# Optimization experiments

Hardware: AMD Instinct MI355X
Metric: run time of the kernel (lower is better)

## Reference

```python
import math
import jax, jax.numpy as jnp
import numpy as np

# Gemma4Audio config constants
HID = 1024
H = 8
D = HID // H            # 128
CHUNK = 12              # attention_chunk_size
PAST = 13 - 1           # max_past_horizon = context_left - 1
FUT = 0                 # max_future_horizon = context_right
CTX = CHUNK + PAST + FUT  # 24
SOFTCAP = 50.0
Q_SCALE = D ** (-0.5) / math.log(2)
K_SCALE = math.log(1.0 + math.e) / math.log(2)


def setup_inputs() -> dict:
    key = jax.random.key(0)
    ks = jax.random.split(key, 8)
    B, S = 4, 6144
    P = CTX + 1  # 25 relative positions
    std = HID ** (-0.5)
    return {
        "hidden_states": jax.random.normal(ks[0], (B, S, HID), jnp.float32),
        "position_embeddings": jax.random.normal(ks[1], (P, HID), jnp.float32),
        "Wq": jax.random.normal(ks[2], (HID, HID), jnp.float32) * std,
        "Wk": jax.random.normal(ks[3], (HID, HID), jnp.float32) * std,
        "Wv": jax.random.normal(ks[4], (HID, HID), jnp.float32) * std,
        "Wpost": jax.random.normal(ks[5], (HID, HID), jnp.float32) * std,
        "Wrel": jax.random.normal(ks[6], (HID, HID), jnp.float32) * std,
        "per_dim_scale": jnp.zeros((D,), jnp.float32),  # torch init: zeros
    }


def _extract_block_context(x, num_blocks):
    # x: [B, S, H, D] -> [B, num_blocks, CTX, H, D]
    xp = jnp.pad(x, ((0, 0), (PAST, FUT + CHUNK - 1), (0, 0), (0, 0)))
    idx = jnp.arange(num_blocks)[:, None] * CHUNK + jnp.arange(CTX)[None, :]
    return xp[:, idx]  # gather along seq axis


def _rel_shift(x):
    # x: [B, H, nb, CHUNK, P] -> [B, H, nb, CHUNK, CTX]
    B, Hh, nb, bs, pos_len = x.shape
    x = jnp.pad(x, ((0, 0), (0, 0), (0, 0), (0, 0), (0, CTX + 1 - pos_len)))
    x = x.reshape(B, Hh, nb, bs * (CTX + 1))[..., : bs * CTX]
    return x.reshape(B, Hh, nb, bs, CTX)


def reference(hidden_states, position_embeddings, Wq, Wk, Wv, Wpost, Wrel, per_dim_scale):
    B, S, _ = hidden_states.shape
    nb = (S + CHUNK - 1) // CHUNK
    pad = nb * CHUNK - S

    # Projections (ClippableLinear clamps are +/-inf at init -> identity)
    q = (hidden_states @ Wq.T).reshape(B, S, H, D)
    k = (hidden_states @ Wk.T).reshape(B, S, H, D)
    v = (hidden_states @ Wv.T).reshape(B, S, H, D)

    q = q * (Q_SCALE * jax.nn.softplus(per_dim_scale))  # per-dim scaled queries
    k = k * K_SCALE

    # [B, nb, CHUNK, H, D]
    q_blocked = jnp.pad(q, ((0, 0), (0, pad), (0, 0), (0, 0))).reshape(B, nb, CHUNK, H, D)
    k_ctx = _extract_block_context(k, nb)  # [B, nb, CTX, H, D]
    v_ctx = _extract_block_context(v, nb)

    # content score: [B, H, nb, CHUNK, CTX]
    matrix_ac = jnp.einsum('bnchd,bnkhd->bhnck', q_blocked, k_ctx)

    # relative position score
    rel_k = (position_embeddings @ Wrel.T).reshape(-1, H, D)  # [P, H, D]
    matrix_bd = jnp.einsum('bnchd,phd->bhncp', q_blocked, rel_k)
    matrix_bd = _rel_shift(matrix_bd)  # [B, H, nb, CHUNK, CTX]

    logits = matrix_ac + matrix_bd
    logits = jnp.tanh(logits / SOFTCAP) * SOFTCAP  # softcap
    attn = jax.nn.softmax(logits, axis=-1)

    out = jnp.einsum('bhnck,bnkhd->bnchd', attn, v_ctx)
    out = out.reshape(B, nb * CHUNK, H * D)[:, :S]
    return out @ Wpost.T
```

## Files before the change

kernel.cpp:

```cpp
#include <hip/hip_runtime.h>
#include <hip/hip_bf16.h>
#include <math.h>

typedef unsigned short ushort_t;
typedef __attribute__((ext_vector_type(8))) short short8;
typedef __attribute__((ext_vector_type(4))) short s4v;
typedef __attribute__((ext_vector_type(4))) float float4v;

#define HID 1024
#define NH 8
#define DH 128
#define CHUNK 12
#define PAST 12
#define CTX 24
#define NPOS 25
#define QKVW 3072

__device__ __forceinline__ float bf2f(ushort_t b){
  union{unsigned int u; float f;} x; x.u = ((unsigned int)b)<<16; return x.f;
}
__device__ __forceinline__ ushort_t f2bf(float f){
  union{float f; unsigned int u;} x; x.f = f;
  unsigned int u = x.u;
  unsigned int r = u + 0x7fffu + ((u>>16)&1u);
  return (ushort_t)(r>>16);
}

__device__ __forceinline__ void gload16(const ushort_t* g, ushort_t* l){
  __builtin_amdgcn_global_load_lds(
      (const __attribute__((address_space(1))) unsigned int*)g,
      (__attribute__((address_space(3))) unsigned int*)l,
      16, 0, 0);
}

__global__ __launch_bounds__(256) void cvt_all(
    const float* __restrict__ hs, const float* __restrict__ Wq,
    const float* __restrict__ Wk, const float* __restrict__ Wv,
    const float* __restrict__ Wp, ushort_t* __restrict__ hsb,
    ushort_t* __restrict__ Wcat, ushort_t* __restrict__ Wpb, int nhs4)
{
  const int W4 = 262144;
  const int total = nhs4 + 4*W4;
  for (int i = blockIdx.x*256 + threadIdx.x; i < total; i += gridDim.x*256){
    const float4v* src; s4v* dst; int off;
    if (i < nhs4){ src = (const float4v*)hs; dst = (s4v*)hsb; off = i; }
    else {
      int j = i - nhs4; int seg = j >> 18; off = j & (W4-1);
      src = (const float4v*)(seg==0?Wq:seg==1?Wk:seg==2?Wv:Wp);
      dst = (seg<3) ? ((s4v*)Wcat) + (size_t)seg*W4 : (s4v*)Wpb;
    }
    float4v v = src[off];
    s4v o;
#pragma unroll
    for (int j2=0;j2<4;j2++) o[j2] = (short)f2bf(v[j2]);
    dst[off] = o;
  }
}

template<int MODE, int OUTF>
__global__ __launch_bounds__(256) void gemm3(
    const ushort_t* __restrict__ A, const ushort_t* __restrict__ W,
    void* __restrict__ Cv, int M, int N, int K,
    const float* __restrict__ pds, float qsc, float ksc)
{
  const int nwg  = gridDim.x;
  const int orig = blockIdx.x;
  const int qch  = nwg >> 3, rch = nwg & 7;
  const int xcd  = orig & 7, idx = orig >> 3;
  const int bid  = (xcd < rch ? xcd*(qch+1) : rch*(qch+1) + (xcd-rch)*qch) + idx;

  const int NT = N >> 7;
  const int m0 = (bid / NT) * 128;
  const int n0 = (bid % NT) * 128;

  const int tid  = threadIdx.x;
  const int w    = tid >> 6, lane = tid & 63;
  const int wm   = w >> 1, wn = w & 1;
  const int lr   = lane & 15;
  const int lg   = lane >> 4;

  __shared__ ushort_t slab[6*128*32];
  ushort_t* a0 = slab;                 ushort_t* b0 = slab + 128*32;
  ushort_t* a1 = slab + 2*128*32;      ushort_t* b1 = slab + 3*128*32;
  ushort_t* a2 = slab + 4*128*32;      ushort_t* b2 = slab + 5*128*32;

  float4v acc[4][4];
#pragma unroll
  for (int i=0;i<4;i++)
#pragma unroll
    for (int j=0;j<4;j++) acc[i][j] = (float4v)0.0f;

  const int sr = ((lane >> 3) << 1) | ((lane >> 2) & 1);
  const int sc = ((lane & 3) ^ ((lane >> 3) & 3)) * 8;

  const int fidx = ((lr >> 1)*8 + (lr & 1)*4 + (lg ^ ((lr >> 1) & 3))) * 8;

  const ushort_t* Ab0 = A + (size_t)(m0 + w*16      + sr)*K + sc;
  const ushort_t* Ab1 = A + (size_t)(m0 + 64 + w*16 + sr)*K + sc;
  const ushort_t* Bb0 = W + (size_t)(n0 + w*16      + sr)*K + sc;
  const ushort_t* Bb1 = W + (size_t)(n0 + 64 + w*16 + sr)*K + sc;

#define STAGE(Abuf, Bbuf, kt) do {                    \
    gload16(Ab0 + (kt), &(Abuf)[(w*16)*32]);          \
    gload16(Ab1 + (kt), &(Abuf)[(64 + w*16)*32]);     \
    gload16(Bb0 + (kt), &(Bbuf)[(w*16)*32]);          \
    gload16(Bb1 + (kt), &(Bbuf)[(64 + w*16)*32]);     \
  } while(0)

#define COMPUTE(Abuf, Bbuf) do {                                             \
    short8 afr[4], bfr[4];                                                   \
    _Pragma("unroll")                                                        \
    for (int i=0;i<4;i++) afr[i] = *(const short8*)&(Abuf)[(wm*4 + i)*512 + fidx]; \
    _Pragma("unroll")                                                        \
    for (int j=0;j<4;j++) bfr[j] = *(const short8*)&(Bbuf)[(wn*4 + j)*512 + fidx]; \
    __builtin_amdgcn_s_setprio(1);                                           \
    _Pragma("unroll")                                                        \
    for (int i=0;i<4;i++)                                                    \
      _Pragma("unroll")                                                      \
      for (int j=0;j<4;j++)                                                  \
        acc[i][j] = __builtin_amdgcn_mfma_f32_16x16x32_bf16(afr[i], bfr[j], acc[i][j], 0,0,0); \
    __builtin_amdgcn_s_setprio(0);                                           \
  } while(0)

  const int nt = K >> 5;
  STAGE(a0, b0, 0);
  STAGE(a1, b1, 32);

  for (int t = 0; t < nt; ++t){
    if (t == nt-1) asm volatile("s_waitcnt vmcnt(0)" ::: "memory");
    else           asm volatile("s_waitcnt vmcnt(4)" ::: "memory");
    asm volatile("s_barrier" ::: "memory");
    if (t+2 < nt) STAGE(a2, b2, (t+2)*32);
    COMPUTE(a0, b0);
    ushort_t* ta = a0; a0 = a1; a1 = a2; a2 = ta;
    ushort_t* tb = b0; b0 = b1; b1 = b2; b2 = tb;
  }
#undef STAGE
#undef COMPUTE

  __syncthreads();

  if (OUTF == 0){
#pragma unroll
    for (int j=0;j<4;j++){
      const int col = wn*64 + j*16 + lr;
      float scale = 1.0f;
      if (MODE==1){
        const int gcol = n0 + col;
        if (gcol < 1024){ float p = pds[gcol & (DH-1)]; scale = qsc * log1pf(expf(p)); }
        else if (gcol < 2048) scale = ksc;
      }
#pragma unroll
      for (int i=0;i<4;i++){
        const int row = wm*64 + i*16 + lg*4;
#pragma unroll
        for (int r=0;r<4;r++)
          slab[(row + r)*128 + col] = f2bf(acc[i][j][r] * scale);
      }
    }
    __syncthreads();
    ushort_t* Crow = (ushort_t*)Cv + (size_t)m0*N + n0;
    const int rr = tid >> 4, sl = (tid & 15)*8;
#pragma unroll
    for (int it=0; it<8; ++it){
      const int row = it*16 + rr;
      *(short8*)&Crow[(size_t)row*N + sl] = *(const short8*)&slab[row*128 + sl];
    }
  } else {
    float* smf = (float*)slab;
    float* Crow = (float*)Cv + (size_t)m0*N + n0;
#pragma unroll
    for (int h2=0; h2<2; ++h2){
      __syncthreads();
      if (wm == h2){
#pragma unroll
        for (int j=0;j<4;j++){
          const int col = wn*64 + j*16 + lr;
#pragma unroll
          for (int i=0;i<4;i++){
            const int row = i*16 + lg*4;
#pragma unroll
            for (int r=0;r<4;r++)
              smf[(row + r)*128 + col] = acc[i][j][r];
          }
        }
      }
      __syncthreads();
      const int rr = tid >> 5, half = ((tid >> 4) & 1)*64, sl = (tid & 15)*4;
#pragma unroll
      for (int it=0; it<8; ++it){
        const int row = it*8 + rr;
        *(float4v*)&Crow[(size_t)(h2*64 + row)*N + half + sl] =
            *(const float4v*)&smf[row*128 + half + sl];
      }
    }
  }
}

__global__ __launch_bounds__(256) void relk2(
    const float* __restrict__ pe, const float* __restrict__ Wrel,
    ushort_t* __restrict__ rel)
{
  int g = blockIdx.x*256 + threadIdx.x;
  int idx = g >> 1, par = g & 1;
  if (idx >= NPOS*HID) return;
  int p = idx >> 10, n = idx & 1023;
  const float* a = pe + p*HID + par*512;
  const float* w = Wrel + (size_t)n*HID + par*512;
  float s = 0.f;
  for (int k=0;k<512;k+=4){
    float4v av = *(const float4v*)(a+k);
    float4v wv = *(const float4v*)(w+k);
#pragma unroll
    for (int u=0;u<4;u++) s += av[u]*wv[u];
  }
  s += __shfl_xor(s, 1, 64);
  if (!par) rel[idx] = f2bf(s);
}

__global__ __launch_bounds__(256) void attn_kernel(
  const ushort_t* __restrict__ qkv, const ushort_t* __restrict__ rel,
  ushort_t* __restrict__ o, int S)
{
  const int n0 = blockIdx.x * 4;
  const int b  = blockIdx.y, h = blockIdx.z;
  const int tid = threadIdx.x;
  const size_t bS = (size_t)b * S;

  __shared__ ushort_t lds[24800];
  ushort_t* ks = lds;
  ushort_t* vt = lds + 9248;
  float*    sB = (float*)(lds + 17952);
  ushort_t* rs = lds + 20448;
  float*    sA = (float*)(lds + 20448);

  const int base = n0*CHUNK - PAST;
  {
    const int r0 = tid >> 4;
    const int c0 = (tid & 15) * 8;
    for (int r = r0; r < 68; r += 16){
      int s = base + r;
      short8 kv = (short8)0, vv = (short8)0;
      if (r < 60 && s >= 0 && s < S){
        kv = *(const short8*)&qkv[(bS + s)*QKVW + 1024 + h*DH + c0];
        vv = *(const short8*)&qkv[(bS + s)*QKVW + 2048 + h*DH + c0];
      }
      *(short8*)&ks[r*136 + c0] = kv;
#pragma unroll
      for (int u=0;u<8;u++) vt[(c0+u)*68 + r] = (ushort_t)vv[u];
    }
    for (int r = r0; r < 32; r += 16){
      short8 rv = (short8)0;
      if (r < NPOS) rv = *(const short8*)&rel[r*HID + h*DH + c0];
      *(short8*)&rs[r*136 + c0] = rv;
    }
  }
  __syncthreads();

  const int w    = tid >> 6;
  const int lane = tid & 63;
  const int lr   = lane & 15;
  const int lg   = lane >> 4;

  float*    sAw = sA + w*312;
  float*    sBw = sB + w*312;
  ushort_t* Ppw = lds + w*640;

  int qrow = (n0 + w)*CHUNK + lr;
  if (qrow >= S) qrow = S - 1;
  const ushort_t* qp = qkv + (bS + qrow)*QKVW + h*DH + lg*8;
  short8 qf[4];
#pragma unroll
  for (int ks2=0; ks2<4; ks2++) qf[ks2] = *(const short8*)(qp + ks2*32);

#pragma unroll
  for (int t0=0; t0<2; t0++){
    float4v acc = (float4v)0.0f;
#pragma unroll
    for (int ks2=0; ks2<4; ks2++){
      short8 rf = *(const short8*)&rs[(t0*16 + lr)*136 + ks2*32 + lg*8];
      acc = __builtin_amdgcn_mfma_f32_16x16x32_bf16(qf[ks2], rf, acc, 0,0,0);
    }
    const int p = t0*16 + lr;
#pragma unroll
    for (int reg=0; reg<4; reg++){
      int cr = lg*4 + reg;
      if (cr < CHUNK && p < NPOS) sBw[cr*26 + p] = acc[reg];
    }
  }
  __syncthreads();

#pragma unroll
  for (int t0=0; t0<2; t0++){
    float4v acc = (float4v)0.0f;
#pragma unroll
    for (int ks2=0; ks2<4; ks2++){
      short8 kf = *(const short8*)&ks[(w*CHUNK + t0*16 + lr)*136 + ks2*32 + lg*8];
      acc = __builtin_amdgcn_mfma_f32_16x16x32_bf16(qf[ks2], kf, acc, 0,0,0);
    }
    const int t = t0*16 + lr;
#pragma unroll
    for (int reg=0; reg<4; reg++){
      int cr = lg*4 + reg;
      if (cr < CHUNK && t < CTX) sAw[cr*26 + t] = acc[reg];
    }
  }
  __syncthreads();

  if (lane < CHUNK) *(short8*)&Ppw[lane*40 + 24] = (short8)0;

  {
    const int c2 = lane >> 5;
    const int t  = lane & 31;
#pragma unroll
    for (int i=0;i<6;i++){
      int c = i*2 + c2;
      float x = -1e30f;
      if (t < CTX){
        int f = c*CTX + t;
        int r = f / NPOS, p = f - r*NPOS;
        x = sAw[c*26 + t] + sBw[r*26 + p];
        x = 50.0f * tanhf(x * 0.02f);
      }
      float m = x;
      for (int off=16; off>=1; off>>=1) m = fmaxf(m, __shfl_xor(m, off, 32));
      float e = (t < CTX) ? expf(x - m) : 0.0f;
      float s = e;
      for (int off=16; off>=1; off>>=1) s += __shfl_xor(s, off, 32);
      if (t < CTX) Ppw[c*40 + t] = f2bf(e / s);
    }
  }

  short8 pf = *(const short8*)&Ppw[lr*40 + lg*8];
  const int orow_base = (n0 + w)*CHUNK;
#pragma unroll
  for (int j=0; j<8; j++){
    int d  = j*16 + lr;
    int tb = w*CHUNK + lg*8;
    s4v b0 = *(const s4v*)&vt[d*68 + tb];
    s4v b1 = *(const s4v*)&vt[d*68 + tb + 4];
    short8 bf;
#pragma unroll
    for (int u=0;u<4;u++){ bf[u] = b0[u]; bf[u+4] = b1[u]; }
    float4v a = __builtin_amdgcn_mfma_f32_16x16x32_bf16(pf, bf, (float4v)0.0f, 0,0,0);
#pragma unroll
    for (int reg=0; reg<4; reg++){
      int cr = lg*4 + reg;
      if (cr < CHUNK)
        o[(bS + orow_base + cr)*HID + h*DH + j*16 + lr] = f2bf(a[reg]);
    }
  }
}

extern "C" void kernel_launch(void* const* d_in, const int* in_sizes, int n_in,
                              void* d_out, int out_size, void* d_ws, size_t ws_size,
                              hipStream_t stream)
{
  const float* hs    = (const float*)d_in[0];
  const float* pe    = (const float*)d_in[1];
  const float* Wq    = (const float*)d_in[2];
  const float* Wk    = (const float*)d_in[3];
  const float* Wv    = (const float*)d_in[4];
  const float* Wpost = (const float*)d_in[5];
  const float* Wrel  = (const float*)d_in[6];
  const float* pds   = (const float*)d_in[7];
  float* out = (float*)d_out;

  const int BS = in_sizes[0] / HID;
  const int B  = 4;
  const int S  = BS / B;
  const int nb = S / CHUNK;

  const size_t per = (size_t)BS * HID;
  const size_t wsz = (size_t)HID * HID;
  ushort_t* qkv  = (ushort_t*)d_ws;
  ushort_t* at   = qkv  + (size_t)BS * QKVW;
  ushort_t* rel  = at   + per;
  ushort_t* hsb  = rel  + (size_t)NPOS*HID;
  ushort_t* Wcat = hsb  + per;
  ushort_t* Wpb  = Wcat + 3*wsz;

  const float qsc = (float)(pow((double)DH, -0.5) / log(2.0));
  const float ksc = (float)(log(1.0 + exp(1.0)) / log(2.0));

  cvt_all<<<4096, 256, 0, stream>>>(hs, Wq, Wk, Wv, Wpost, hsb, Wcat, Wpb,
                                    (int)(per/4));
  relk2<<<200, 256, 0, stream>>>(pe, Wrel, rel);

  gemm3<1,0><<<(BS/128)*(QKVW/128), 256, 0, stream>>>(
      hsb, Wcat, qkv, BS, QKVW, HID, pds, qsc, ksc);
  attn_kernel<<<dim3(nb/4, B, NH), 256, 0, stream>>>(qkv, rel, at, S);
  gemm3<0,1><<<(BS/128)*(HID/128), 256, 0, stream>>>(
      at, Wpb, out, BS, HID, HID, nullptr, 1.0f, 1.0f);
}
```

Baseline: 383.0 us.

## Add 256x128-tile GEMM kernel for the fused QKV projection

Adds a new GEMM kernel, used for the QKV projection, in which each workgroup computes a 256x128 output tile. Each wave holds an 8x4 grid of MFMA accumulators, reuses its B fragments across eight A rows, and keeps triple-buffered LDS staging. The epilogue stages the scaled bf16 results through LDS so the global stores are coalesced. This raises arithmetic intensity per LDS load and halves the workgroup count, at the cost of more accumulator registers and LDS, which may lower occupancy. The `sr` expression in the existing GEMM is rewritten into an equivalent simpler form.

```diff
diff --git a/kernel.cpp b/kernel.cpp
--- a/kernel.cpp
+++ b/kernel.cpp
@@ -57,6 +57,120 @@
   }
 }
 
+template<int MODE>
+__global__ __launch_bounds__(256) void gemmw(
+    const ushort_t* __restrict__ A, const ushort_t* __restrict__ W,
+    ushort_t* __restrict__ C, int M, int N, int K,
+    const float* __restrict__ pds, float qsc, float ksc)
+{
+  const int nwg  = gridDim.x;
+  const int orig = blockIdx.x;
+  const int qch  = nwg >> 3, rch = nwg & 7;
+  const int xcd  = orig & 7, idx = orig >> 3;
+  const int bid  = (xcd < rch ? xcd*(qch+1) : rch*(qch+1) + (xcd-rch)*qch) + idx;
+
+  const int NT = N >> 7;
+  const int m0 = (bid / NT) * 256;
+  const int n0 = (bid % NT) * 128;
+
+  const int tid  = threadIdx.x;
+  const int w    = tid >> 6, lane = tid & 63;
+  const int wm   = w >> 1, wn = w & 1;
+  const int lr   = lane & 15;
+  const int lg   = lane >> 4;
+
+  __shared__ ushort_t slab[3*12288];
+  ushort_t* a0 = slab;              ushort_t* b0 = slab + 8192;
+  ushort_t* a1 = slab + 12288;      ushort_t* b1 = slab + 20480;
+  ushort_t* a2 = slab + 24576;      ushort_t* b2 = slab + 32768;
+
+  float4v acc[8][4];
+#pragma unroll
+  for (int i=0;i<8;i++)
+#pragma unroll
+    for (int j=0;j<4;j++) acc[i][j] = (float4v)0.0f;
+
+  const int sr = lane >> 2;
+  const int sc = ((lane & 3) ^ ((lane >> 3) & 3)) * 8;
+  const int ps = (lg ^ ((lr >> 1) & 3)) * 8;
+
+  const ushort_t* Ag0 = A + (size_t)(m0 +       w*16 + sr)*K + sc;
+  const ushort_t* Ag1 = A + (size_t)(m0 +  64 + w*16 + sr)*K + sc;
+  const ushort_t* Ag2 = A + (size_t)(m0 + 128 + w*16 + sr)*K + sc;
+  const ushort_t* Ag3 = A + (size_t)(m0 + 192 + w*16 + sr)*K + sc;
+  const ushort_t* Bg0 = W + (size_t)(n0 +       w*16 + sr)*K + sc;
+  const ushort_t* Bg1 = W + (size_t)(n0 +  64 + w*16 + sr)*K + sc;
+
+#define STAGE(Abuf, Bbuf, kt) do {                      \
+    gload16(Ag0 + (kt), &(Abuf)[(      w*16)*32]);      \
+    gload16(Ag1 + (kt), &(Abuf)[( 64 + w*16)*32]);      \
+    gload16(Ag2 + (kt), &(Abuf)[(128 + w*16)*32]);      \
+    gload16(Ag3 + (kt), &(Abuf)[(192 + w*16)*32]);      \
+    gload16(Bg0 + (kt), &(Bbuf)[(      w*16)*32]);      \
+    gload16(Bg1 + (kt), &(Bbuf)[( 64 + w*16)*32]);      \
+  } while(0)
+
+#define COMPUTE(Abuf, Bbuf) do {                                             \
+    short8 bfr[4];                                                           \
+    _Pragma("unroll")                                                        \
+    for (int j=0;j<4;j++)                                                    \
+      bfr[j] = *(const short8*)&(Bbuf)[(wn*64 + j*16 + lr)*32 + ps];         \
+    __builtin_amdgcn_s_setprio(1);                                           \
+    _Pragma("unroll")                                                        \
+    for (int mi=0; mi<8; mi++){                                              \
+      short8 afr = *(const short8*)&(Abuf)[(wm*128 + mi*16 + lr)*32 + ps];   \
+      _Pragma("unroll")                                                      \
+      for (int j=0;j<4;j++)                                                  \
+        acc[mi][j] = __builtin_amdgcn_mfma_f32_16x16x32_bf16(afr, bfr[j], acc[mi][j], 0,0,0); \
+    }                                                                        \
+    __builtin_amdgcn_s_setprio(0);                                           \
+  } while(0)
+
+  const int nt = K >> 5;
+  STAGE(a0, b0, 0);
+  STAGE(a1, b1, 32);
+
+  for (int t = 0; t < nt; ++t){
+    if (t == nt-1) asm volatile("s_waitcnt vmcnt(0)" ::: "memory");
+    else           asm volatile("s_waitcnt vmcnt(6)" ::: "memory");
+    asm volatile("s_barrier" ::: "memory");
+    if (t+2 < nt) STAGE(a2, b2, (t+2)*32);
+    COMPUTE(a0, b0);
+    ushort_t* ta = a0; a0 = a1; a1 = a2; a2 = ta;
+    ushort_t* tb = b0; b0 = b1; b1 = b2; b2 = tb;
+  }
+#undef STAGE
+#undef COMPUTE
+
+  __syncthreads();
+
+#pragma unroll
+  for (int j=0;j<4;j++){
+    const int col = wn*64 + j*16 + lr;
+    float scale = 1.0f;
+    if (MODE==1){
+      const int gcol = n0 + col;
+      if (gcol < 1024){ float p = pds[gcol & (DH-1)]; scale = qsc * log1pf(expf(p)); }
+      else if (gcol < 2048) scale = ksc;
+    }
+#pragma unroll
+    for (int mi=0; mi<8; mi++){
+      const int row = wm*128 + mi*16 + lg*4;
+#pragma unroll
+      for (int r=0;r<4;r++)
+        slab[(row + r)*128 + col] = f2bf(acc[mi][j][r] * scale);
+    }
+  }
+  __syncthreads();
+  ushort_t* Crow = C + (size_t)m0*N + n0;
+  const int rr = tid >> 4, sl = (tid & 15)*8;
+#pragma unroll
+  for (int it=0; it<16; ++it){
+    const int row = it*16 + rr;
+    *(short8*)&Crow[(size_t)row*N + sl] = *(const short8*)&slab[row*128 + sl];
+  }
+}
+
 template<int MODE, int OUTF>
 __global__ __launch_bounds__(256) void gemm3(
     const ushort_t* __restrict__ A, const ushort_t* __restrict__ W,
@@ -90,9 +204,8 @@
 #pragma unroll
     for (int j=0;j<4;j++) acc[i][j] = (float4v)0.0f;
 
-  const int sr = ((lane >> 3) << 1) | ((lane >> 2) & 1);
+  const int sr = lane >> 2;
   const int sc = ((lane & 3) ^ ((lane >> 3) & 3)) * 8;
-
   const int fidx = ((lr >> 1)*8 + (lr & 1)*4 + (lg ^ ((lr >> 1) & 3))) * 8;
 
   const ushort_t* Ab0 = A + (size_t)(m0 + w*16      + sr)*K + sc;
@@ -387,7 +500,7 @@
                                     (int)(per/4));
   relk2<<<200, 256, 0, stream>>>(pe, Wrel, rel);
 
-  gemm3<1,0><<<(BS/128)*(QKVW/128), 256, 0, stream>>>(
+  gemmw<1><<<(BS/256)*(QKVW/128), 256, 0, stream>>>(
       hsb, Wcat, qkv, BS, QKVW, HID, pds, qsc, ksc);
   attn_kernel<<<dim3(nb/4, B, NH), 256, 0, stream>>>(qkv, rel, at, S);
   gemm3<0,1><<<(BS/128)*(HID/128), 256, 0, stream>>>(
```

Result: slower. 401.2 us (+4.8%).
